# Performance work log

Hardware: AMD Instinct MI355X
Metric: run time of the kernel (lower is better)

Reference implementation:

```python
import jax, jax.numpy as jnp
import numpy as np

N = 100000      # nodes
E = 1600000     # edges (avg degree 16)
IN = 128        # in_channels
HID = 128       # hidden_channels
OUT = 2         # out_channels
NEG_SLOPE = 0.2  # PyG GATConv default


def setup_inputs() -> dict:
    key = jax.random.key(0)
    ks = jax.random.split(key, 20)
    inp = {
        "x": jax.random.normal(ks[0], (N, IN), dtype=jnp.float32),
        "edge_index": jax.random.randint(ks[1], (2, E), 0, N, dtype=jnp.int32),
    }
    # GATConv params (heads=1): W:[din,dout], attention vecs a_src/a_dst:[dout], bias:[dout]
    dims = [(IN, HID), (HID, HID), (HID, HID)]
    for i, (din, dout) in enumerate(dims, start=1):
        base = 4 * i
        inp[f"W{i}"] = jax.random.normal(ks[base], (din, dout), dtype=jnp.float32) * (1.0 / np.sqrt(din))
        inp[f"a{i}s"] = jax.random.normal(ks[base + 1], (dout,), dtype=jnp.float32) * 0.1
        inp[f"a{i}d"] = jax.random.normal(ks[base + 2], (dout,), dtype=jnp.float32) * 0.1
        inp[f"b{i}"] = jnp.zeros((dout,), dtype=jnp.float32)
    inp["Wc"] = jax.random.normal(ks[16], (HID, OUT), dtype=jnp.float32) * (1.0 / np.sqrt(HID))
    inp["bc"] = jnp.zeros((OUT,), dtype=jnp.float32)
    return inp


def _gat_layer(x, src, dst, W, a_s, a_d, b, n):
    # Linear transform: [n, dout]
    h = x @ W
    # Edge attention logits: alpha_src[j] + alpha_dst[i], LeakyReLU (PyG GATConv)
    e = jax.nn.leaky_relu(jnp.take(h @ a_s, src) + jnp.take(h @ a_d, dst), NEG_SLOPE)
    # Stable softmax over incoming edges per destination node
    m = jax.ops.segment_max(e, dst, num_segments=n)
    ex = jnp.exp(e - m[dst])
    denom = jax.ops.segment_sum(ex, dst, num_segments=n)
    alpha = ex / denom[dst]
    # Weighted scatter-aggregation of source features into destinations
    out = jax.ops.segment_sum(alpha[:, None] * jnp.take(h, src, axis=0), dst, num_segments=n)
    return out + b


def reference(x, edge_index, W1, a1s, a1d, b1, W2, a2s, a2d, b2, W3, a3s, a3d, b3, Wc, bc):
    n = x.shape[0]
    # PyG GATConv default add_self_loops=True
    loop = jnp.arange(n, dtype=edge_index.dtype)
    src = jnp.concatenate([edge_index[0], loop])
    dst = jnp.concatenate([edge_index[1], loop])
    for (W, a_s, a_d, b) in ((W1, a1s, a1d, b1), (W2, a2s, a2d, b2), (W3, a3s, a3d, b3)):
        x = jax.nn.relu(_gat_layer(x, src, dst, W, a_s, a_d, b, n))
    return x @ Wc + bc
```

## Files before the change

kernel.cpp:

```cpp
#include <hip/hip_runtime.h>
#include <hip/hip_fp16.h>

#define NNODES 100000
#define NEDGES 1600000
#define DIM 128
#define NB ((NNODES + 63) / 64)
#define NCH 128
#define CHUNK ((NEDGES + NCH - 1) / NCH)
#define EBUF 2560
#define LSTR 136
#define NSL16 ((size_t)NNODES * 16)
#define CSRSZ (NEDGES + NB * 256 + 64)

typedef _Float16 f16x8 __attribute__((ext_vector_type(8)));
typedef float f32x4 __attribute__((ext_vector_type(4)));

__device__ __forceinline__ float leaky02(float t) { return t > 0.f ? t : 0.2f * t; }

union H8u { uint2 u; __half2 h[2]; };


__global__ __launch_bounds__(256) void wprep(const float* __restrict__ W0,
                                             const float* __restrict__ W1,
                                             const float* __restrict__ W2,
                                             __half* __restrict__ wt) {
    int idx = blockIdx.x * 256 + threadIdx.x;
    if (idx >= 3 * 128 * 128) return;
    int l = idx >> 14, rem = idx & 16383;
    int nn = rem >> 7, k = rem & 127;
    const float* W = (l == 0) ? W0 : ((l == 1) ? W1 : W2);
    wt[idx] = __float2half_rn(W[k * 128 + nn]);
}

template <bool XF16>
__global__ __launch_bounds__(256) void gemm_mfma(const float* __restrict__ X,
                                                 const __half* __restrict__ X16,
                                                 const __half* __restrict__ wt16,
                                                 const float* __restrict__ as_,
                                                 const float* __restrict__ ad_,
                                                 __half* __restrict__ H,
                                                 float* __restrict__ s,
                                                 float* __restrict__ d, int n) {
    __shared__ __half As[64][LSTR];
    __shared__ __half Wt[128][LSTR];
    int t = threadIdx.x;
    int brow = blockIdx.x * 64;

    if (XF16) {
        for (int i = t; i < 64 * 16; i += 256) {
            int r = i >> 4, c8 = (i & 15) * 8;
            int gr = brow + r;
            int sl = c8 >> 4, off = c8 & 15;
            uint4 v = (gr < n) ? *(const uint4*)(X16 + (size_t)sl * NSL16 + (size_t)gr * 16 + off)
                               : make_uint4(0u, 0u, 0u, 0u);
            *(uint4*)&As[r][c8] = v;
        }
    } else {
        for (int i = t; i < 64 * 32; i += 256) {
            int r = i >> 5, c4 = (i & 31) * 4;
            int gr = brow + r;
            float4 v = (gr < n) ? *(const float4*)(X + (size_t)gr * 128 + c4)
                                : make_float4(0.f, 0.f, 0.f, 0.f);
            As[r][c4 + 0] = __float2half_rn(v.x);
            As[r][c4 + 1] = __float2half_rn(v.y);
            As[r][c4 + 2] = __float2half_rn(v.z);
            As[r][c4 + 3] = __float2half_rn(v.w);
        }
    }
    for (int i = t; i < 128 * 16; i += 256) {
        int r = i >> 4, c8 = (i & 15) * 8;
        *(uint4*)&Wt[r][c8] = *(const uint4*)(wt16 + r * 128 + c8);
    }
    __syncthreads();

    int wid  = t >> 6;
    int lane = t & 63;
    int lrow = lane & 15;
    int lkg  = lane >> 4;
    int r0   = wid * 16;

    f32x4 acc[8] = {};
#pragma unroll
    for (int kk = 0; kk < 128; kk += 32) {
        f16x8 af = *(const f16x8*)&As[r0 + lrow][kk + lkg * 8];
#pragma unroll
        for (int ct = 0; ct < 8; ++ct) {
            f16x8 bf = *(const f16x8*)&Wt[ct * 16 + lrow][kk + lkg * 8];
            acc[ct] = __builtin_amdgcn_mfma_f32_16x16x32_f16(af, bf, acc[ct], 0, 0, 0);
        }
    }

    float sp[4] = {0.f, 0.f, 0.f, 0.f};
    float dp[4] = {0.f, 0.f, 0.f, 0.f};
#pragma unroll
    for (int ct = 0; ct < 8; ++ct) {
        float a_s = as_[ct * 16 + lrow];
        float a_d = ad_[ct * 16 + lrow];
#pragma unroll
        for (int j = 0; j < 4; ++j) {
            sp[j] += acc[ct][j] * a_s;
            dp[j] += acc[ct][j] * a_d;
        }
    }
#pragma unroll
    for (int j = 0; j < 4; ++j) {
        int gr = brow + r0 + lkg * 4 + j;
        if (gr < n) {
#pragma unroll
            for (int ct = 0; ct < 8; ++ct)
                H[(size_t)ct * NSL16 + (size_t)gr * 16 + lrow] = __float2half_rn(acc[ct][j]);
        }
    }
#pragma unroll
    for (int off = 1; off < 16; off <<= 1)
#pragma unroll
        for (int j = 0; j < 4; ++j) {
            sp[j] += __shfl_xor(sp[j], off);
            dp[j] += __shfl_xor(dp[j], off);
        }
    if (lrow == 0)
#pragma unroll
        for (int j = 0; j < 4; ++j) {
            int gr = brow + r0 + lkg * 4 + j;
            if (gr < n) { s[gr] = sp[j]; d[gr] = dp[j]; }
        }
}

__global__ __launch_bounds__(512) void bucket_count(const int* __restrict__ dst,
                                                    int* __restrict__ blockcounts) {
    __shared__ int hist[NB];
    int b = blockIdx.x, t = threadIdx.x;
    for (int i = t; i < NB; i += 512) hist[i] = 0;
    __syncthreads();
    int e0 = b * CHUNK, e1 = min(NEDGES, e0 + CHUNK);
    for (int e = e0 + t; e < e1; e += 512)
        atomicAdd(&hist[dst[e] >> 6], 1);
    __syncthreads();
    for (int i = t; i < NB; i += 512)
        blockcounts[i * NCH + b] = hist[i];
}

__global__ __launch_bounds__(NCH) void bucket_scan_a(int* __restrict__ blockcounts,
                                                     int* __restrict__ btotal) {
    int bin = blockIdx.x, t = threadIdx.x;
    int v = blockcounts[bin * NCH + t];
    int incl = v;
#pragma unroll
    for (int off = 1; off < 64; off <<= 1) {
        int u = __shfl_up(incl, off, 64);
        if ((t & 63) >= off) incl += u;
    }
    __shared__ int wsum;
    if (t == 63) wsum = incl;
    __syncthreads();
    int excl = incl - v + ((t >= 64) ? wsum : 0);
    blockcounts[bin * NCH + t] = excl;
    if (t == NCH - 1) btotal[bin] = excl + v;
}

__global__ __launch_bounds__(1024) void bucket_scan_b(const int* __restrict__ btotal,
                                                      int* __restrict__ bbase) {
    __shared__ int ts[2][1024];
    int t = threadIdx.x;
    int b0 = t * 2;
    int c0 = (b0 < NB)     ? btotal[b0]     : 0;
    int c1 = (b0 + 1 < NB) ? btotal[b0 + 1] : 0;
    int sum = c0 + c1;
    ts[0][t] = sum;
    __syncthreads();
    int sb = 0;
    for (int off = 1; off < 1024; off <<= 1) {
        int v = ts[sb][t] + ((t >= off) ? ts[sb][t - off] : 0);
        ts[sb ^ 1][t] = v;
        sb ^= 1;
        __syncthreads();
    }
    int excl = ts[sb][t] - sum;
    if (b0 < NB)     bbase[b0]     = excl;
    if (b0 + 1 < NB) bbase[b0 + 1] = excl + c0;
    if (t == 1023) bbase[NB] = ts[sb][1023];
}

__global__ __launch_bounds__(512) void bucket_scatter(const int* __restrict__ src,
                                                      const int* __restrict__ dst,
                                                      const int* __restrict__ blockcounts,
                                                      const int* __restrict__ bbase,
                                                      int* __restrict__ packed) {
    __shared__ int cur[NB];
    int b = blockIdx.x, t = threadIdx.x;
    for (int i = t; i < NB; i += 512) cur[i] = bbase[i] + blockcounts[i * NCH + b];
    __syncthreads();
    int e0 = b * CHUNK, e1 = min(NEDGES, e0 + CHUNK);
    for (int e = e0 + t; e < e1; e += 512) {
        int dv = dst[e];
        int bin = dv >> 6;
        int p = atomicAdd(&cur[bin], 1);
        packed[p] = ((dv & 63) << 17) | src[e];
    }
}

__global__ __launch_bounds__(256) void bucket_csr(const int* __restrict__ packed,
                                                  const int* __restrict__ bbase,
                                                  int* __restrict__ rowptr4,
                                                  int* __restrict__ cnts,
                                                  int* __restrict__ csr_src) {
    __shared__ int ebuf[EBUF];
    __shared__ int hist[64], cur[64];
    int i = blockIdx.x, t = threadIdx.x;
    int base_in = bbase[i], cnt = bbase[i + 1] - base_in;
    int pbase = ((base_in + 3) & ~3) + i * 256;
    bool inl = (cnt <= EBUF);
    if (inl) for (int j = t; j < cnt; j += 256) ebuf[j] = packed[base_in + j];
    if (t < 64) hist[t] = 0;
    __syncthreads();
    for (int j = t; j < cnt; j += 256) {
        int v = inl ? ebuf[j] : packed[base_in + j];
        atomicAdd(&hist[v >> 17], 1);
    }
    __syncthreads();
    if (t < 64) {
        int node = i * 64 + t;
        bool valid = node < NNODES;
        int h = hist[t];
        int c  = h + (valid ? 1 : 0);
        int c4 = (c + 3) & ~3;
        int incl = c4;
#pragma unroll
        for (int off = 1; off < 64; off <<= 1) {
            int u = __shfl_up(incl, off, 64);
            if (t >= off) incl += u;
        }
        int ex4 = incl - c4;
        cur[t] = pbase + ex4;
        if (valid) {
            rowptr4[node] = pbase + ex4;
            cnts[node] = c;
            csr_src[pbase + ex4 + h] = node;
        }
    }
    __syncthreads();
    for (int j = t; j < cnt; j += 256) {
        int v = inl ? ebuf[j] : packed[base_in + j];
        int off = atomicAdd(&cur[v >> 17], 1);
        csr_src[off] = v & 0x1FFFF;
    }
}

__global__ __launch_bounds__(256) void gat_alpha(const int* __restrict__ rowptr4,
                                                 const int* __restrict__ cnts,
                                                 const int* __restrict__ csr,
                                                 const float* __restrict__ s,
                                                 const float* __restrict__ d,
                                                 unsigned* __restrict__ packed2, int n) {
    int node = blockIdx.x * 8 + (threadIdx.x >> 5);
    if (node >= n) return;
    int lane = threadIdx.x & 31;
    int base = rowptr4[node];
    int cnt  = cnts[node];
    int cnt4 = (cnt + 3) & ~3;
    float dnode = d[node];

    if (cnt <= 32) {
        int si = csr[base + min(lane, cnt - 1)];
        float lv = leaky02(s[si] + dnode);
        float lm = (lane < cnt) ? lv : -1e30f;
#pragma unroll
        for (int off = 16; off; off >>= 1) lm = fmaxf(lm, __shfl_xor(lm, off));
        float w = (lane < cnt) ? expf(lv - lm) : 0.f;
        float denom = w;
#pragma unroll
        for (int off = 16; off; off >>= 1) denom += __shfl_xor(denom, off);
        if (lane < cnt)
            packed2[base + lane] = ((unsigned)si << 15) |
                                   (unsigned)__float2int_rn(w / denom * 32767.f);
        else if (lane < cnt4)
            packed2[base + lane] = (unsigned)node << 15;
    } else {
        float m = -1e30f;
        for (int c = 0; c < cnt; c += 32) {
            int idx = c + lane;
            float lv = (idx < cnt) ? leaky02(s[csr[base + idx]] + dnode) : -1e30f;
            m = fmaxf(m, lv);
        }
#pragma unroll
        for (int off = 16; off; off >>= 1) m = fmaxf(m, __shfl_xor(m, off));
        float denom = 0.f;
        for (int c = 0; c < cnt; c += 32) {
            int idx = c + lane;
            if (idx < cnt) denom += expf(leaky02(s[csr[base + idx]] + dnode) - m);
        }
#pragma unroll
        for (int off = 16; off; off >>= 1) denom += __shfl_xor(denom, off);
        for (int c = 0; c < cnt4; c += 32) {
            int idx = c + lane;
            if (idx < cnt) {
                int si = csr[base + idx];
                float w = expf(leaky02(s[si] + dnode) - m);
                packed2[base + idx] = ((unsigned)si << 15) |
                                      (unsigned)__float2int_rn(w / denom * 32767.f);
            } else if (idx < cnt4) {
                packed2[base + idx] = (unsigned)node << 15;
            }
        }
    }
}

__global__ __launch_bounds__(256) void gat_agg(const int* __restrict__ rowptr4,
                                               const int* __restrict__ cnts,
                                               const unsigned* __restrict__ packed2,
                                               const __half* __restrict__ H,
                                               const float* __restrict__ bias,
                                               __half* __restrict__ A16, int n) {
    int sl  = blockIdx.x & 7;
    int blk = blockIdx.x >> 3;
    int wid = threadIdx.x >> 6;
    int lane = threadIdx.x & 63;
    int nd = lane >> 2;
    int cq = lane & 3;
    int node = blk * 64 + wid * 16 + nd;
    if (node >= n) return;
    const __half* Hs = H + (size_t)sl * NSL16 + cq * 4;
    __half* As = A16 + (size_t)sl * NSL16;

    int base  = rowptr4[node];
    int iters = (cnts[node] + 3) >> 2;
    const unsigned* p = packed2 + base;
    f32x4 acc = {0.f, 0.f, 0.f, 0.f};
    for (int it = 0; it < iters; ++it) {
        uint2 qa = *(const uint2*)(p + it * 4);
        uint2 qb = *(const uint2*)(p + it * 4 + 2);
        unsigned pk0 = qa.x, pk1 = qa.y, pk2 = qb.x, pk3 = qb.y;
        float a0 = (float)(pk0 & 0x7fffu);
        float a1 = (float)(pk1 & 0x7fffu);
        float a2 = (float)(pk2 & 0x7fffu);
        float a3 = (float)(pk3 & 0x7fffu);
        H8u h0, h1, h2, h3;
        h0.u = *(const uint2*)(Hs + (size_t)(pk0 >> 15) * 16);
        h1.u = *(const uint2*)(Hs + (size_t)(pk1 >> 15) * 16);
        h2.u = *(const uint2*)(Hs + (size_t)(pk2 >> 15) * 16);
        h3.u = *(const uint2*)(Hs + (size_t)(pk3 >> 15) * 16);
        float2 p00 = __half22float2(h0.h[0]), p01 = __half22float2(h0.h[1]);
        float2 p10 = __half22float2(h1.h[0]), p11 = __half22float2(h1.h[1]);
        float2 p20 = __half22float2(h2.h[0]), p21 = __half22float2(h2.h[1]);
        float2 p30 = __half22float2(h3.h[0]), p31 = __half22float2(h3.h[1]);
        acc[0] += a0 * p00.x + a1 * p10.x + a2 * p20.x + a3 * p30.x;
        acc[1] += a0 * p00.y + a1 * p10.y + a2 * p20.y + a3 * p30.y;
        acc[2] += a0 * p01.x + a1 * p11.x + a2 * p21.x + a3 * p31.x;
        acc[3] += a0 * p01.y + a1 * p11.y + a2 * p21.y + a3 * p31.y;
    }
    const float scale = 1.f / 32767.f;
    float o0 = fmaxf(acc[0] * scale + bias[sl * 16 + cq * 4 + 0], 0.f);
    float o1 = fmaxf(acc[1] * scale + bias[sl * 16 + cq * 4 + 1], 0.f);
    float o2 = fmaxf(acc[2] * scale + bias[sl * 16 + cq * 4 + 2], 0.f);
    float o3 = fmaxf(acc[3] * scale + bias[sl * 16 + cq * 4 + 3], 0.f);
    H8u pk16;
    pk16.h[0] = __floats2half2_rn(o0, o1);
    pk16.h[1] = __floats2half2_rn(o2, o3);
    *(uint2*)(As + (size_t)node * 16 + cq * 4) = pk16.u;
}

__global__ __launch_bounds__(256) void classify16(const __half* __restrict__ A,
                                                  const float* __restrict__ Wc,
                                                  const float* __restrict__ bc,
                                                  float* __restrict__ out, int n) {
    int node = blockIdx.x * 4 + (threadIdx.x >> 6);
    if (node >= n) return;
    int lane = threadIdx.x & 63;
    int col = lane * 2;
    int sl = col >> 4, off = col & 15;
    __half2 h2 = *(const __half2*)(A + (size_t)sl * NSL16 + (size_t)node * 16 + off);
    float2 f = __half22float2(h2);
    float o0 = f.x * Wc[col * 2]       + f.y * Wc[(col + 1) * 2];
    float o1 = f.x * Wc[col * 2 + 1]   + f.y * Wc[(col + 1) * 2 + 1];
#pragma unroll
    for (int offx = 32; offx; offx >>= 1) {
        o0 += __shfl_xor(o0, offx);
        o1 += __shfl_xor(o1, offx);
    }
    if (lane == 0) {
        out[(size_t)node * 2 + 0] = o0 + bc[0];
        out[(size_t)node * 2 + 1] = o1 + bc[1];
    }
}

extern "C" void kernel_launch(void* const* d_in, const int* in_sizes, int n_in,
                              void* d_out, int out_size, void* d_ws, size_t ws_size,
                              hipStream_t stream) {
    const float* x   = (const float*)d_in[0];
    const int*   ei  = (const int*)d_in[1];
    const int*   src = ei;
    const int*   dst = ei + NEDGES;
    const float* Ws[3]  = {(const float*)d_in[2], (const float*)d_in[6], (const float*)d_in[10]};
    const float* ass[3] = {(const float*)d_in[3], (const float*)d_in[7], (const float*)d_in[11]};
    const float* ads[3] = {(const float*)d_in[4], (const float*)d_in[8], (const float*)d_in[12]};
    const float* bs[3]  = {(const float*)d_in[5], (const float*)d_in[9], (const float*)d_in[13]};
    const float* Wc = (const float*)d_in[14];
    const float* bc = (const float*)d_in[15];
    float* out = (float*)d_out;

    const int n = NNODES;

    __half*   h16  = (__half*)d_ws;
    __half*   a16  = h16 + (size_t)n * DIM;
    __half*   wt16 = a16 + (size_t)n * DIM;
    float*    sbuf = (float*)(wt16 + 3 * 128 * 128);
    float*    dbuf = sbuf + n;
    int*      rowptr4     = (int*)(dbuf + n);
    int*      cnts        = rowptr4 + n;
    int*      csr_src     = cnts + n;
    unsigned* packed2     = (unsigned*)(csr_src + CSRSZ);
    int*      packed      = (int*)(packed2 + CSRSZ);
    int*      blockcounts = packed + NEDGES;
    int*      bbase       = blockcounts + NB * NCH;
    int*      btotal      = bbase + NB + 1;

    const int g64        = (n + 63) / 64;
    const int alpha_grid = (n + 7) / 8;
    const int cls_grid   = (n + 3) / 4;
    const int agg_grid   = ((n + 63) / 64) * 8;

    wprep<<<192, 256, 0, stream>>>(Ws[0], Ws[1], Ws[2], wt16);
    bucket_count<<<NCH, 512, 0, stream>>>(dst, blockcounts);
    bucket_scan_a<<<NB, NCH, 0, stream>>>(blockcounts, btotal);
    bucket_scan_b<<<1, 1024, 0, stream>>>(btotal, bbase);
    bucket_scatter<<<NCH, 512, 0, stream>>>(src, dst, blockcounts, bbase, packed);
    bucket_csr<<<NB, 256, 0, stream>>>(packed, bbase, rowptr4, cnts, csr_src);

    for (int layer = 0; layer < 3; ++layer) {
        const __half* wl = wt16 + (size_t)layer * 128 * 128;
        if (layer == 0)
            gemm_mfma<false><<<g64, 256, 0, stream>>>(x, a16, wl, ass[0], ads[0],
                                                      h16, sbuf, dbuf, n);
        else
            gemm_mfma<true><<<g64, 256, 0, stream>>>(x, a16, wl, ass[layer], ads[layer],
                                                     h16, sbuf, dbuf, n);
        gat_alpha<<<alpha_grid, 256, 0, stream>>>(rowptr4, cnts, csr_src, sbuf, dbuf,
                                                  packed2, n);
        gat_agg<<<agg_grid, 256, 0, stream>>>(rowptr4, cnts, packed2, h16, bs[layer], a16, n);
    }
    classify16<<<cls_grid, 256, 0, stream>>>(a16, Wc, bc, out, n);
}
```

Measured before the change: 431.9 us.

## Sort nodes by degree bucket for aggregation and prefetch packed edge words

Adds a node_sort kernel that groups nodes within each 1024-node segment by their padded in-degree, so the 16 nodes sharing a wavefront in gat_agg have similar loop trip counts and less divergence. gat_agg now reads its node through this order array. It also loads the four packed edge entries as one uint4 and software-prefetches the next group. The cost is one extra small kernel, an indirection per node, scattered output writes, and a prefetch read that runs one uint4 past each node's edge list.

```diff
diff --git a/kernel.cpp b/kernel.cpp
--- a/kernel.cpp
+++ b/kernel.cpp
@@ -246,6 +246,30 @@
     }
 }
 
+__global__ __launch_bounds__(256) void node_sort(const int* __restrict__ cnts,
+                                                 int* __restrict__ order, int n) {
+    __shared__ int hist[16], curb[16];
+    int seg = blockIdx.x, t = threadIdx.x;
+    int n0 = seg * 1024, n1 = min(n, n0 + 1024);
+    if (t < 16) hist[t] = 0;
+    __syncthreads();
+    for (int i = n0 + t; i < n1; i += 256) {
+        int b = min(((cnts[i] + 3) >> 2) - 1, 15);
+        atomicAdd(&hist[b], 1);
+    }
+    __syncthreads();
+    if (t == 0) {
+        int run = 0;
+        for (int b = 0; b < 16; ++b) { curb[b] = run; run += hist[b]; }
+    }
+    __syncthreads();
+    for (int i = n0 + t; i < n1; i += 256) {
+        int b = min(((cnts[i] + 3) >> 2) - 1, 15);
+        int p = atomicAdd(&curb[b], 1);
+        order[n0 + p] = i;
+    }
+}
+
 __global__ __launch_bounds__(256) void gat_alpha(const int* __restrict__ rowptr4,
                                                  const int* __restrict__ cnts,
                                                  const int* __restrict__ csr,
@@ -307,6 +331,7 @@
 
 __global__ __launch_bounds__(256) void gat_agg(const int* __restrict__ rowptr4,
                                                const int* __restrict__ cnts,
+                                               const int* __restrict__ order,
                                                const unsigned* __restrict__ packed2,
                                                const __half* __restrict__ H,
                                                const float* __restrict__ bias,
@@ -317,28 +342,28 @@
     int lane = threadIdx.x & 63;
     int nd = lane >> 2;
     int cq = lane & 3;
-    int node = blk * 64 + wid * 16 + nd;
-    if (node >= n) return;
+    int idx = blk * 64 + wid * 16 + nd;
+    if (idx >= n) return;
+    int node = order[idx];
     const __half* Hs = H + (size_t)sl * NSL16 + cq * 4;
     __half* As = A16 + (size_t)sl * NSL16;
 
     int base  = rowptr4[node];
     int iters = (cnts[node] + 3) >> 2;
-    const unsigned* p = packed2 + base;
+    const uint4* p = (const uint4*)(packed2 + base);
     f32x4 acc = {0.f, 0.f, 0.f, 0.f};
+    uint4 q = p[0];
     for (int it = 0; it < iters; ++it) {
-        uint2 qa = *(const uint2*)(p + it * 4);
-        uint2 qb = *(const uint2*)(p + it * 4 + 2);
-        unsigned pk0 = qa.x, pk1 = qa.y, pk2 = qb.x, pk3 = qb.y;
-        float a0 = (float)(pk0 & 0x7fffu);
-        float a1 = (float)(pk1 & 0x7fffu);
-        float a2 = (float)(pk2 & 0x7fffu);
-        float a3 = (float)(pk3 & 0x7fffu);
+        uint4 nq = p[it + 1];
+        float a0 = (float)(q.x & 0x7fffu);
+        float a1 = (float)(q.y & 0x7fffu);
+        float a2 = (float)(q.z & 0x7fffu);
+        float a3 = (float)(q.w & 0x7fffu);
         H8u h0, h1, h2, h3;
-        h0.u = *(const uint2*)(Hs + (size_t)(pk0 >> 15) * 16);
-        h1.u = *(const uint2*)(Hs + (size_t)(pk1 >> 15) * 16);
-        h2.u = *(const uint2*)(Hs + (size_t)(pk2 >> 15) * 16);
-        h3.u = *(const uint2*)(Hs + (size_t)(pk3 >> 15) * 16);
+        h0.u = *(const uint2*)(Hs + (size_t)(q.x >> 15) * 16);
+        h1.u = *(const uint2*)(Hs + (size_t)(q.y >> 15) * 16);
+        h2.u = *(const uint2*)(Hs + (size_t)(q.z >> 15) * 16);
+        h3.u = *(const uint2*)(Hs + (size_t)(q.w >> 15) * 16);
         float2 p00 = __half22float2(h0.h[0]), p01 = __half22float2(h0.h[1]);
         float2 p10 = __half22float2(h1.h[0]), p11 = __half22float2(h1.h[1]);
         float2 p20 = __half22float2(h2.h[0]), p21 = __half22float2(h2.h[1]);
@@ -347,6 +372,7 @@
         acc[1] += a0 * p00.y + a1 * p10.y + a2 * p20.y + a3 * p30.y;
         acc[2] += a0 * p01.x + a1 * p11.x + a2 * p21.x + a3 * p31.x;
         acc[3] += a0 * p01.y + a1 * p11.y + a2 * p21.y + a3 * p31.y;
+        q = nq;
     }
     const float scale = 1.f / 32767.f;
     float o0 = fmaxf(acc[0] * scale + bias[sl * 16 + cq * 4 + 0], 0.f);
@@ -407,7 +433,8 @@
     float*    dbuf = sbuf + n;
     int*      rowptr4     = (int*)(dbuf + n);
     int*      cnts        = rowptr4 + n;
-    int*      csr_src     = cnts + n;
+    int*      order       = cnts + n;
+    int*      csr_src     = order + n;
     unsigned* packed2     = (unsigned*)(csr_src + CSRSZ);
     int*      packed      = (int*)(packed2 + CSRSZ);
     int*      blockcounts = packed + NEDGES;
@@ -418,6 +445,7 @@
     const int alpha_grid = (n + 7) / 8;
     const int cls_grid   = (n + 3) / 4;
     const int agg_grid   = ((n + 63) / 64) * 8;
+    const int sort_grid  = (n + 1023) / 1024;
 
     wprep<<<192, 256, 0, stream>>>(Ws[0], Ws[1], Ws[2], wt16);
     bucket_count<<<NCH, 512, 0, stream>>>(dst, blockcounts);
@@ -425,6 +453,7 @@
     bucket_scan_b<<<1, 1024, 0, stream>>>(btotal, bbase);
     bucket_scatter<<<NCH, 512, 0, stream>>>(src, dst, blockcounts, bbase, packed);
     bucket_csr<<<NB, 256, 0, stream>>>(packed, bbase, rowptr4, cnts, csr_src);
+    node_sort<<<sort_grid, 256, 0, stream>>>(cnts, order, n);
 
     for (int layer = 0; layer < 3; ++layer) {
         const __half* wl = wt16 + (size_t)layer * 128 * 128;
@@ -436,7 +465,8 @@
                                                      h16, sbuf, dbuf, n);
         gat_alpha<<<alpha_grid, 256, 0, stream>>>(rowptr4, cnts, csr_src, sbuf, dbuf,
                                                   packed2, n);
-        gat_agg<<<agg_grid, 256, 0, stream>>>(rowptr4, cnts, packed2, h16, bs[layer], a16, n);
+        gat_agg<<<agg_grid, 256, 0, stream>>>(rowptr4, cnts, order, packed2, h16,
+                                              bs[layer], a16, n);
     }
     classify16<<<cls_grid, 256, 0, stream>>>(a16, Wc, bc, out, n);
 }
```

New measurement: 477.4 us. 10.5% more time.

## Regroup feature layout into 32-column slices and widen aggregation gathers

Applied to the files above, without the earlier changes.

Changes the sliced half-precision feature layout from eight 16-column slices to four 32-column groups, updating the GEMM store/load, aggregation and classifier indexing. Each aggregation lane now gathers 8 halves (16 bytes) per neighbor, and the grid covers 4 groups instead of 8, so the edge list is re-read half as often. Also software-prefetches the next packed edge quad. This trades more registers per thread and fewer blocks for wider, less redundant memory traffic.

```diff
diff --git a/kernel.cpp b/kernel.cpp
--- a/kernel.cpp
+++ b/kernel.cpp
@@ -9,7 +9,7 @@
 #define CHUNK ((NEDGES + NCH - 1) / NCH)
 #define EBUF 2560
 #define LSTR 136
-#define NSL16 ((size_t)NNODES * 16)
+#define NGR32 ((size_t)NNODES * 32)
 #define CSRSZ (NEDGES + NB * 256 + 64)
 
 typedef _Float16 f16x8 __attribute__((ext_vector_type(8)));
@@ -17,7 +17,8 @@
 
 __device__ __forceinline__ float leaky02(float t) { return t > 0.f ? t : 0.2f * t; }
 
-union H8u { uint2 u; __half2 h[2]; };
+union H8u  { uint2 u; __half2 h[2]; };
+union H16u { uint4 u; __half2 h[4]; };
 
 
 __global__ __launch_bounds__(256) void wprep(const float* __restrict__ W0,
@@ -50,8 +51,8 @@
         for (int i = t; i < 64 * 16; i += 256) {
             int r = i >> 4, c8 = (i & 15) * 8;
             int gr = brow + r;
-            int sl = c8 >> 4, off = c8 & 15;
-            uint4 v = (gr < n) ? *(const uint4*)(X16 + (size_t)sl * NSL16 + (size_t)gr * 16 + off)
+            int g = c8 >> 5, off = c8 & 31;
+            uint4 v = (gr < n) ? *(const uint4*)(X16 + (size_t)g * NGR32 + (size_t)gr * 32 + off)
                                : make_uint4(0u, 0u, 0u, 0u);
             *(uint4*)&As[r][c8] = v;
         }
@@ -108,7 +109,8 @@
         if (gr < n) {
 #pragma unroll
             for (int ct = 0; ct < 8; ++ct)
-                H[(size_t)ct * NSL16 + (size_t)gr * 16 + lrow] = __float2half_rn(acc[ct][j]);
+                H[(size_t)(ct >> 1) * NGR32 + (size_t)gr * 32 + (ct & 1) * 16 + lrow] =
+                    __float2half_rn(acc[ct][j]);
         }
     }
 #pragma unroll
@@ -311,52 +313,54 @@
                                                const __half* __restrict__ H,
                                                const float* __restrict__ bias,
                                                __half* __restrict__ A16, int n) {
-    int sl  = blockIdx.x & 7;
-    int blk = blockIdx.x >> 3;
+    int grp = blockIdx.x & 3;
+    int blk = blockIdx.x >> 2;
     int wid = threadIdx.x >> 6;
     int lane = threadIdx.x & 63;
     int nd = lane >> 2;
-    int cq = lane & 3;
+    int cg = lane & 3;
     int node = blk * 64 + wid * 16 + nd;
     if (node >= n) return;
-    const __half* Hs = H + (size_t)sl * NSL16 + cq * 4;
-    __half* As = A16 + (size_t)sl * NSL16;
+    const __half* Hs = H + (size_t)grp * NGR32 + cg * 8;
+    __half* As = A16 + (size_t)grp * NGR32;
 
     int base  = rowptr4[node];
     int iters = (cnts[node] + 3) >> 2;
-    const unsigned* p = packed2 + base;
-    f32x4 acc = {0.f, 0.f, 0.f, 0.f};
+    const uint4* p = (const uint4*)(packed2 + base);
+    float acc[8] = {0.f, 0.f, 0.f, 0.f, 0.f, 0.f, 0.f, 0.f};
+    uint4 q = p[0];
     for (int it = 0; it < iters; ++it) {
-        uint2 qa = *(const uint2*)(p + it * 4);
-        uint2 qb = *(const uint2*)(p + it * 4 + 2);
-        unsigned pk0 = qa.x, pk1 = qa.y, pk2 = qb.x, pk3 = qb.y;
-        float a0 = (float)(pk0 & 0x7fffu);
-        float a1 = (float)(pk1 & 0x7fffu);
-        float a2 = (float)(pk2 & 0x7fffu);
-        float a3 = (float)(pk3 & 0x7fffu);
-        H8u h0, h1, h2, h3;
-        h0.u = *(const uint2*)(Hs + (size_t)(pk0 >> 15) * 16);
-        h1.u = *(const uint2*)(Hs + (size_t)(pk1 >> 15) * 16);
-        h2.u = *(const uint2*)(Hs + (size_t)(pk2 >> 15) * 16);
-        h3.u = *(const uint2*)(Hs + (size_t)(pk3 >> 15) * 16);
-        float2 p00 = __half22float2(h0.h[0]), p01 = __half22float2(h0.h[1]);
-        float2 p10 = __half22float2(h1.h[0]), p11 = __half22float2(h1.h[1]);
-        float2 p20 = __half22float2(h2.h[0]), p21 = __half22float2(h2.h[1]);
-        float2 p30 = __half22float2(h3.h[0]), p31 = __half22float2(h3.h[1]);
-        acc[0] += a0 * p00.x + a1 * p10.x + a2 * p20.x + a3 * p30.x;
-        acc[1] += a0 * p00.y + a1 * p10.y + a2 * p20.y + a3 * p30.y;
-        acc[2] += a0 * p01.x + a1 * p11.x + a2 * p21.x + a3 * p31.x;
-        acc[3] += a0 * p01.y + a1 * p11.y + a2 * p21.y + a3 * p31.y;
+        uint4 nq = p[it + 1];
+        float a0 = (float)(q.x & 0x7fffu);
+        float a1 = (float)(q.y & 0x7fffu);
+        float a2 = (float)(q.z & 0x7fffu);
+        float a3 = (float)(q.w & 0x7fffu);
+        H16u h0, h1, h2, h3;
+        h0.u = *(const uint4*)(Hs + (size_t)(q.x >> 15) * 32);
+        h1.u = *(const uint4*)(Hs + (size_t)(q.y >> 15) * 32);
+        h2.u = *(const uint4*)(Hs + (size_t)(q.z >> 15) * 32);
+        h3.u = *(const uint4*)(Hs + (size_t)(q.w >> 15) * 32);
+#pragma unroll
+        for (int c2 = 0; c2 < 4; ++c2) {
+            float2 f0 = __half22float2(h0.h[c2]);
+            float2 f1 = __half22float2(h1.h[c2]);
+            float2 f2 = __half22float2(h2.h[c2]);
+            float2 f3 = __half22float2(h3.h[c2]);
+            acc[c2 * 2 + 0] += a0 * f0.x + a1 * f1.x + a2 * f2.x + a3 * f3.x;
+            acc[c2 * 2 + 1] += a0 * f0.y + a1 * f1.y + a2 * f2.y + a3 * f3.y;
+        }
+        q = nq;
     }
     const float scale = 1.f / 32767.f;
-    float o0 = fmaxf(acc[0] * scale + bias[sl * 16 + cq * 4 + 0], 0.f);
-    float o1 = fmaxf(acc[1] * scale + bias[sl * 16 + cq * 4 + 1], 0.f);
-    float o2 = fmaxf(acc[2] * scale + bias[sl * 16 + cq * 4 + 2], 0.f);
-    float o3 = fmaxf(acc[3] * scale + bias[sl * 16 + cq * 4 + 3], 0.f);
-    H8u pk16;
-    pk16.h[0] = __floats2half2_rn(o0, o1);
-    pk16.h[1] = __floats2half2_rn(o2, o3);
-    *(uint2*)(As + (size_t)node * 16 + cq * 4) = pk16.u;
+    int cb = grp * 32 + cg * 8;
+    H16u pk16;
+#pragma unroll
+    for (int c2 = 0; c2 < 4; ++c2) {
+        float o0 = fmaxf(acc[c2 * 2 + 0] * scale + bias[cb + c2 * 2 + 0], 0.f);
+        float o1 = fmaxf(acc[c2 * 2 + 1] * scale + bias[cb + c2 * 2 + 1], 0.f);
+        pk16.h[c2] = __floats2half2_rn(o0, o1);
+    }
+    *(uint4*)(As + (size_t)node * 32 + cg * 8) = pk16.u;
 }
 
 __global__ __launch_bounds__(256) void classify16(const __half* __restrict__ A,
@@ -367,8 +371,8 @@
     if (node >= n) return;
     int lane = threadIdx.x & 63;
     int col = lane * 2;
-    int sl = col >> 4, off = col & 15;
-    __half2 h2 = *(const __half2*)(A + (size_t)sl * NSL16 + (size_t)node * 16 + off);
+    int g = col >> 5, off = col & 31;
+    __half2 h2 = *(const __half2*)(A + (size_t)g * NGR32 + (size_t)node * 32 + off);
     float2 f = __half22float2(h2);
     float o0 = f.x * Wc[col * 2]       + f.y * Wc[(col + 1) * 2];
     float o1 = f.x * Wc[col * 2 + 1]   + f.y * Wc[(col + 1) * 2 + 1];
@@ -417,7 +421,7 @@
     const int g64        = (n + 63) / 64;
     const int alpha_grid = (n + 7) / 8;
     const int cls_grid   = (n + 3) / 4;
-    const int agg_grid   = ((n + 63) / 64) * 8;
+    const int agg_grid   = ((n + 63) / 64) * 4;
 
     wprep<<<192, 256, 0, stream>>>(Ws[0], Ws[1], Ws[2], wt16);
     bucket_count<<<NCH, 512, 0, stream>>>(dst, blockcounts);
```

Result: faster. 403.1 us (-6.7%).
